# Optimization experiments

Hardware: AMD Instinct MI355X
Metric: run time of the kernel (lower is better)

## Reference

```python
import jax, jax.numpy as jnp
import numpy as np

DMODEL = 512
NUM_HEADS = 8
HEAD_DIM = DMODEL // NUM_HEADS
ATTN_LEN = 5
BATCH = 4
SEQ = 4096


def kv_roll(t, layer, shift):
    # t: [B, h_sub, T, 1, hd]; replicates tf.pad + tf.roll + concat + slice
    T = t.shape[2]
    dil = 2 ** layer
    p = dil * (ATTN_LEN // 2)
    tp = jnp.pad(t, ((0, 0), (0, 0), (p, p), (0, 0), (0, 0)))
    # circular rolls, concat along the singleton window axis -> [B,h,T+2p,ATTN_LEN,hd]
    rolled = jnp.concatenate(
        [jnp.roll(tp, -i * dil, axis=2) for i in range(shift, ATTN_LEN + shift)],
        axis=3,
    )
    return rolled[:, :, :T]


def setup_inputs() -> dict:
    key = jax.random.key(0)
    ks = jax.random.split(key, 8)
    inputs = jax.random.normal(ks[0], (BATCH, SEQ, DMODEL), dtype=jnp.float32)
    Wq = jax.random.normal(ks[1], (DMODEL, DMODEL), dtype=jnp.float32) * 0.02
    bq = jnp.zeros((DMODEL,), dtype=jnp.float32)
    Wk = jax.random.normal(ks[2], (DMODEL, DMODEL), dtype=jnp.float32) * 0.02
    bk = jnp.zeros((DMODEL,), dtype=jnp.float32)
    Wv = jax.random.normal(ks[3], (DMODEL, DMODEL), dtype=jnp.float32) * 0.02
    bv = jnp.zeros((DMODEL,), dtype=jnp.float32)
    Er = jax.random.normal(ks[4], (NUM_HEADS, HEAD_DIM, ATTN_LEN), dtype=jnp.float32) * 0.05
    return {"inputs": inputs, "Wq": Wq, "bq": bq, "Wk": Wk, "bk": bk,
            "Wv": Wv, "bv": bv, "Er": Er, "layer": 1}


def reference(inputs, Wq, bq, Wk, bk, Wv, bv, Er, layer):
    B, T, D = inputs.shape
    # projections -> [B, H, T, 1, hd]
    def proj(W, b):
        x = inputs @ W + b
        x = x.reshape(B, T, NUM_HEADS, 1, HEAD_DIM)
        return jnp.transpose(x, (0, 2, 1, 3, 4))
    q = proj(Wq, bq)
    k = proj(Wk, bk)
    v = proj(Wv, bv)

    def build_windows(t):
        # per-head-group shifts: heads 0-3 shift 0, head 4 shift -2, head 5 -1, head 6 +1, head 7 +2
        return jnp.concatenate((
            kv_roll(t[:, 0:4], layer, 0),
            kv_roll(t[:, 4:5], layer, -2),
            kv_roll(t[:, 5:6], layer, -1),
            kv_roll(t[:, 6:7], layer, 1),
            kv_roll(t[:, 7:8], layer, 2),
        ), axis=1)  # [B, H, T, ATTN_LEN, hd]

    kw = build_windows(k)
    vw = build_windows(v)

    # qk: [B, H, T, 1, ATTN_LEN]
    qk = jnp.einsum('bhtqd,bhtwd->bhtqw', q, kw)
    # relative positional bias: q @ Er -> [B, H, T, 1, ATTN_LEN]
    qEr = jnp.einsum('bhtqd,hdw->bhtqw', q, Er)
    scale = jnp.sqrt(jnp.float32(HEAD_DIM)).astype(inputs.dtype)
    logits = (qk + qEr) / scale
    mask = (qk == 0).astype(logits.dtype)
    attn = jax.nn.softmax(logits + mask * -10000.0, axis=-1)
    # out: [B, H, T, 1, hd]
    out = jnp.einsum('bhtqw,bhtwd->bhtqd', attn, vw)
    out = jnp.transpose(out[:, :, :, 0, :], (0, 2, 1, 3)).reshape(B, T, D)
    return out, attn
```

## Files before the change

### kernel.cpp

```cpp
#include <hip/hip_runtime.h>
#include <stdint.h>

#define B_ 4
#define T_ 4096
#define D_ 512
#define H_ 8
#define HD_ 64
#define W_ 5
#define M_ (B_*T_)
#define TILE 128
#define HALO 16
#define TMg 160
#define TN 192
#define LSTR 72

#define AS1_OFF 5120
#define BS0_OFF 10240
#define BS1_OFF 16384
#define SH_ELEMS 32256

typedef __attribute__((ext_vector_type(8))) short short8;
typedef __attribute__((ext_vector_type(4))) float floatx4;

__device__ __forceinline__ unsigned short f2bf(float f) {
    unsigned int u = __builtin_bit_cast(unsigned int, f);
    u += 0x7fffu + ((u >> 16) & 1u);
    return (unsigned short)(u >> 16);
}
__device__ __forceinline__ float bf2f(unsigned short s) {
    unsigned int u = ((unsigned int)s) << 16;
    return __builtin_bit_cast(float, u);
}
__device__ __forceinline__ void load8bf(const unsigned short* p, float* f) {
    uint4 d = *(const uint4*)p;
    f[0] = bf2f((unsigned short)(d.x & 0xffffu));
    f[1] = bf2f((unsigned short)(d.x >> 16));
    f[2] = bf2f((unsigned short)(d.y & 0xffffu));
    f[3] = bf2f((unsigned short)(d.y >> 16));
    f[4] = bf2f((unsigned short)(d.z & 0xffffu));
    f[5] = bf2f((unsigned short)(d.z >> 16));
    f[6] = bf2f((unsigned short)(d.w & 0xffffu));
    f[7] = bf2f((unsigned short)(d.w >> 16));
}

__device__ __forceinline__ void async16(const unsigned short* g, unsigned short* l) {
    __builtin_amdgcn_global_load_lds(
        (const __attribute__((address_space(1))) unsigned int*)g,
        (__attribute__((address_space(3))) unsigned int*)l, 16, 0, 0);
}

__global__ __launch_bounds__(256) void prep(const float* __restrict__ x,
                                            const float* __restrict__ Wq,
                                            const float* __restrict__ Wk,
                                            const float* __restrict__ Wv,
                                            unsigned short* __restrict__ xb,
                                            unsigned short* __restrict__ Wt2) {
    int bx = blockIdx.x;
    if (bx < 4096) {
        int i = bx * 256 + threadIdx.x;
        const float4* x4 = (const float4*)x;
        float4 a = x4[2*i], b = x4[2*i + 1];
        uint4 o;
        o.x = (unsigned)f2bf(a.x) | ((unsigned)f2bf(a.y) << 16);
        o.y = (unsigned)f2bf(a.z) | ((unsigned)f2bf(a.w) << 16);
        o.z = (unsigned)f2bf(b.x) | ((unsigned)f2bf(b.y) << 16);
        o.w = (unsigned)f2bf(b.z) | ((unsigned)f2bf(b.w) << 16);
        ((uint4*)xb)[i] = o;
    } else {
        int tid = (bx - 4096) * 256 + threadIdx.x;
        int np = tid % 1536;
        int kc = tid / 1536;
        int h = np / 192, n192 = np % 192;
        int sel = n192 >> 6, ch = n192 & 63;
        int c = h * 64 + ch;
        const float* Wsrc = (sel == 0) ? Wq : ((sel == 1) ? Wk : Wv);
        unsigned short us[8];
#pragma unroll
        for (int j = 0; j < 8; j++)
            us[j] = f2bf(Wsrc[(size_t)(kc*8 + j) * D_ + c]);
        uint4 o;
        o.x = (unsigned)us[0] | ((unsigned)us[1] << 16);
        o.y = (unsigned)us[2] | ((unsigned)us[3] << 16);
        o.z = (unsigned)us[4] | ((unsigned)us[5] << 16);
        o.w = (unsigned)us[6] | ((unsigned)us[7] << 16);
        *(uint4*)(Wt2 + (size_t)np * D_ + kc*8) = o;
    }
}

__global__ __launch_bounds__(512, 4) void fused_qkv_attn(
    const unsigned short* __restrict__ Xb,
    const unsigned short* __restrict__ Wt2,
    const float* __restrict__ bq, const float* __restrict__ bk2,
    const float* __restrict__ bv, const float* __restrict__ Er,
    const int* __restrict__ layer_p,
    float* __restrict__ out,
    float* __restrict__ attn_out)
{
    __shared__ unsigned short SH[SH_ELEMS];
    __shared__ float sEr[HD_ * W_];
    unsigned short* As0 = SH;
    unsigned short* Bs0 = SH + BS0_OFF;
    unsigned short* Qs = SH;
    unsigned short* Ks = SH + TILE * LSTR;
    unsigned short* Vs = SH + (TILE + TMg) * LSTR;

    const int tid = threadIdx.x;
    const int wave = tid >> 6, lane = tid & 63;
    const int tile = blockIdx.x >> 3, h = blockIdx.x & 7;
    const int b = tile >> 5;
    const int t0 = (tile & 31) * TILE;
    const long m0g = (long)b * T_ + t0;

    for (int i = tid; i < HD_ * W_; i += 512)
        sEr[i] = Er[h * HD_ * W_ + i];

    const unsigned short* gsrc[3];
    unsigned short* ldst[3];
    int halfoff[3];
#pragma unroll
    for (int j = 0; j < 3; j++) {
        int q = wave + j * 8;
        if (q < 22) {
            if (q < 10) {
                long grow = m0g - HALO + q*16 + (lane >> 2);
                grow = grow < 0 ? 0 : (grow >= M_ ? M_ - 1 : grow);
                gsrc[j] = Xb + grow * D_ + (lane & 3) * 8;
                ldst[j] = As0 + q * 512;
                halfoff[j] = AS1_OFF;
            } else {
                int q2 = q - 10;
                gsrc[j] = Wt2 + ((size_t)h*TN + q2*16 + (lane >> 2)) * D_ + (lane & 3) * 8;
                ldst[j] = Bs0 + q2 * 512;
                halfoff[j] = BS1_OFF - BS0_OFF;
            }
        }
    }

    const int wm = (wave >> 2) * 80;
    const int wn = (wave & 3) * 48;
    const int qd = lane >> 4, r16 = lane & 15;
    floatx4 acc[5][3] = {};

    for (int kc = 0; kc < D_; kc += 64) {
#pragma unroll
        for (int j = 0; j < 3; j++)
            if (wave + j * 8 < 22) {
                async16(gsrc[j] + kc,      ldst[j]);
                async16(gsrc[j] + kc + 32, ldst[j] + halfoff[j]);
            }
        __syncthreads();
        short8 af[5][2], bf[3][2];
#pragma unroll
        for (int half = 0; half < 2; half++) {
            const unsigned short* Ab = SH + half * AS1_OFF;
            const unsigned short* Bb = SH + BS0_OFF + half * (BS1_OFF - BS0_OFF);
#pragma unroll
            for (int mi = 0; mi < 5; mi++)
                af[mi][half] = __builtin_bit_cast(short8,
                    *(const uint4*)(Ab + (wm + mi*16 + r16)*32 + qd*8));
#pragma unroll
            for (int ni = 0; ni < 3; ni++)
                bf[ni][half] = __builtin_bit_cast(short8,
                    *(const uint4*)(Bb + (wn + ni*16 + r16)*32 + qd*8));
        }
#pragma unroll
        for (int half = 0; half < 2; half++)
#pragma unroll
            for (int mi = 0; mi < 5; mi++)
#pragma unroll
                for (int ni = 0; ni < 3; ni++)
                    acc[mi][ni] = __builtin_amdgcn_mfma_f32_16x16x32_bf16(
                        af[mi][half], bf[ni][half], acc[mi][ni], 0, 0, 0);
        __syncthreads();
    }

#pragma unroll
    for (int ni = 0; ni < 3; ni++) {
        int n192 = wn + ni * 16 + r16;
        int sel = n192 >> 6;
        int ch = n192 & 63;
        float bias = (sel == 0) ? bq[h*64 + ch]
                   : (sel == 1) ? bk2[h*64 + ch] : bv[h*64 + ch];
#pragma unroll
        for (int mi = 0; mi < 5; mi++)
#pragma unroll
            for (int r = 0; r < 4; r++) {
                int l = wm + mi*16 + qd*4 + r;
                unsigned short vb = f2bf(acc[mi][ni][r] + bias);
                if (sel == 0) {
                    if (l >= HALO && l < HALO + TILE)
                        Qs[(l - HALO) * LSTR + ch] = vb;
                } else if (sel == 1) {
                    Ks[l * LSTR + ch] = vb;
                } else {
                    Vs[l * LSTR + ch] = vb;
                }
            }
    }
    __syncthreads();

    const int dil = 1 << layer_p[0];
    const int sh = (h < 4) ? 0 : (h == 4 ? -2 : (h == 5 ? -1 : (h == 6 ? 1 : 2)));
    const int c8 = tid & 7, g64 = tid >> 3;

#pragma unroll
    for (int p = 0; p < 2; p++) {
        int tl = g64 + p * 64;
        int t = t0 + tl;
        float qf[8]; load8bf(Qs + tl * LSTR + c8 * 8, qf);

        int pos[W_]; bool val[W_]; float s[W_];
#pragma unroll
        for (int w = 0; w < W_; w++) {
            pos[w] = t + (sh + w - 2) * dil;
            val[w] = (pos[w] >= 0) && (pos[w] < T_);
            float a = 0.f;
            if (val[w]) {
                float kf[8]; load8bf(Ks + (pos[w] - t0 + HALO) * LSTR + c8 * 8, kf);
#pragma unroll
                for (int j = 0; j < 8; j++) a = fmaf(qf[j], kf[j], a);
            }
#pragma unroll
            for (int j = 0; j < 8; j++)
                a = fmaf(qf[j], sEr[(c8*8 + j) * W_ + w], a);
            s[w] = a;
        }
#pragma unroll
        for (int off = 4; off > 0; off >>= 1)
#pragma unroll
            for (int w = 0; w < W_; w++)
                s[w] += __shfl_xor(s[w], off, 8);

        float logit[W_], mx = -1e30f;
#pragma unroll
        for (int w = 0; w < W_; w++) {
            logit[w] = val[w] ? s[w] * 0.125f : -1e30f;
            mx = fmaxf(mx, logit[w]);
        }
        float pw[W_], ssum = 0.f;
#pragma unroll
        for (int w = 0; w < W_; w++) {
            pw[w] = val[w] ? __expf(logit[w] - mx) : 0.f;
            ssum += pw[w];
        }
        const float inv = 1.f / ssum;
        float aw[W_];
#pragma unroll
        for (int w = 0; w < W_; w++) aw[w] = pw[w] * inv;

        if (c8 < W_)
            attn_out[((size_t)(b * H_ + h) * T_ + t) * W_ + c8] = aw[c8];

        float of[8] = {0,0,0,0,0,0,0,0};
#pragma unroll
        for (int w = 0; w < W_; w++) {
            if (val[w]) {
                float vf[8]; load8bf(Vs + (pos[w] - t0 + HALO) * LSTR + c8 * 8, vf);
#pragma unroll
                for (int j = 0; j < 8; j++) of[j] = fmaf(aw[w], vf[j], of[j]);
            }
        }
        float* orow = out + ((size_t)b * T_ + t) * D_ + h * HD_ + c8 * 8;
        *(float4*)(orow)     = make_float4(of[0], of[1], of[2], of[3]);
        *(float4*)(orow + 4) = make_float4(of[4], of[5], of[6], of[7]);
    }
}

extern "C" void kernel_launch(void* const* d_in, const int* in_sizes, int n_in,
                              void* d_out, int out_size, void* d_ws, size_t ws_size,
                              hipStream_t stream) {
    const float* x   = (const float*)d_in[0];
    const float* Wq  = (const float*)d_in[1];
    const float* bq  = (const float*)d_in[2];
    const float* Wk  = (const float*)d_in[3];
    const float* bk  = (const float*)d_in[4];
    const float* Wv  = (const float*)d_in[5];
    const float* bv  = (const float*)d_in[6];
    const float* Er  = (const float*)d_in[7];
    const int* layer = (const int*)d_in[8];

    char* ws = (char*)d_ws;
    unsigned short* Xb  = (unsigned short*)ws;
    unsigned short* Wt2 = (unsigned short*)(ws + (size_t)16*1024*1024);

    float* out  = (float*)d_out;
    float* attn = out + (size_t)B_ * T_ * D_;

    prep<<<4096 + 384, 256, 0, stream>>>(x, Wq, Wk, Wv, Xb, Wt2);
    fused_qkv_attn<<<(M_ / TILE) * 8, 512, 0, stream>>>(Xb, Wt2, bq, bk, bv,
                                                        Er, layer, out, attn);
}
```

Baseline: 149.4 us.

## Double-buffer activation tiles in LDS and load weight fragments directly from global

The GEMM main loop now double-buffers only the activation (A) tile in shared memory, prefetching the next K-chunk while the current one is consumed. It also drops shared-memory staging of the weight (B) tile: each wave reads its MFMA B fragments straight from global memory. This halves the barriers per iteration and overlaps the async copies with compute, at the cost of more global/L2 traffic for the weights, which several blocks reuse, and possible exposed global-load latency.

```diff
diff --git a/kernel.cpp b/kernel.cpp
--- a/kernel.cpp
+++ b/kernel.cpp
@@ -14,9 +14,8 @@
 #define TN 192
 #define LSTR 72
 
-#define AS1_OFF 5120
-#define BS0_OFF 10240
-#define BS1_OFF 16384
+#define AHALF 5120
+#define ABUF  10240
 #define SH_ELEMS 32256
 
 typedef __attribute__((ext_vector_type(8))) short short8;
@@ -98,8 +97,6 @@
 {
     __shared__ unsigned short SH[SH_ELEMS];
     __shared__ float sEr[HD_ * W_];
-    unsigned short* As0 = SH;
-    unsigned short* Bs0 = SH + BS0_OFF;
     unsigned short* Qs = SH;
     unsigned short* Ks = SH + TILE * LSTR;
     unsigned short* Vs = SH + (TILE + TMg) * LSTR;
@@ -114,63 +111,70 @@
     for (int i = tid; i < HD_ * W_; i += 512)
         sEr[i] = Er[h * HD_ * W_ + i];
 
-    const unsigned short* gsrc[3];
-    unsigned short* ldst[3];
-    int halfoff[3];
+    const unsigned short* agA[3];
+    unsigned short* alA[3];
+    int nA = 0;
 #pragma unroll
     for (int j = 0; j < 3; j++) {
-        int q = wave + j * 8;
-        if (q < 22) {
-            if (q < 10) {
-                long grow = m0g - HALO + q*16 + (lane >> 2);
-                grow = grow < 0 ? 0 : (grow >= M_ ? M_ - 1 : grow);
-                gsrc[j] = Xb + grow * D_ + (lane & 3) * 8;
-                ldst[j] = As0 + q * 512;
-                halfoff[j] = AS1_OFF;
-            } else {
-                int q2 = q - 10;
-                gsrc[j] = Wt2 + ((size_t)h*TN + q2*16 + (lane >> 2)) * D_ + (lane & 3) * 8;
-                ldst[j] = Bs0 + q2 * 512;
-                halfoff[j] = BS1_OFF - BS0_OFF;
-            }
-        }
-    }
-
-    const int wm = (wave >> 2) * 80;
-    const int wn = (wave & 3) * 48;
+        int J = wave + 8 * j;
+        if (J < 20) {
+            int q = J >> 1, hh = J & 1;
+            long grow = m0g - HALO + q*16 + (lane >> 2);
+            grow = grow < 0 ? 0 : (grow >= M_ ? M_ - 1 : grow);
+            agA[nA] = Xb + grow * D_ + hh*32 + (lane & 3) * 8;
+            alA[nA] = SH + hh * AHALF + q * 512 + lane * 8;
+            nA++;
+        }
+    }
+
+    const int wm = (wave >> 2) * 80, wn = (wave & 3) * 48;
     const int qd = lane >> 4, r16 = lane & 15;
+    const unsigned short* bsrc[3];
+#pragma unroll
+    for (int ni = 0; ni < 3; ni++)
+        bsrc[ni] = Wt2 + ((size_t)(h * TN + wn + ni*16 + r16)) * D_ + qd * 8;
+
+#pragma unroll
+    for (int j = 0; j < 3; j++)
+        if (j < nA) async16(agA[j], alA[j]);
+    __syncthreads();
+
     floatx4 acc[5][3] = {};
 
-    for (int kc = 0; kc < D_; kc += 64) {
-#pragma unroll
-        for (int j = 0; j < 3; j++)
-            if (wave + j * 8 < 22) {
-                async16(gsrc[j] + kc,      ldst[j]);
-                async16(gsrc[j] + kc + 32, ldst[j] + halfoff[j]);
-            }
-        __syncthreads();
-        short8 af[5][2], bf[3][2];
-#pragma unroll
-        for (int half = 0; half < 2; half++) {
-            const unsigned short* Ab = SH + half * AS1_OFF;
-            const unsigned short* Bb = SH + BS0_OFF + half * (BS1_OFF - BS0_OFF);
+#pragma unroll
+    for (int it = 0; it < 8; it++) {
+        const int kc = it * 64;
+        const unsigned short* Abuf = SH + (it & 1) * ABUF;
+
+        short8 bf[2][3];
+#pragma unroll
+        for (int hh = 0; hh < 2; hh++)
+#pragma unroll
+            for (int ni = 0; ni < 3; ni++)
+                bf[hh][ni] = __builtin_bit_cast(short8,
+                    *(const uint4*)(bsrc[ni] + kc + hh*32));
+
+        if (it < 7) {
+#pragma unroll
+            for (int j = 0; j < 3; j++)
+                if (j < nA)
+                    async16(agA[j] + kc + 64, alA[j] + ((it + 1) & 1) * ABUF);
+        }
+
+#pragma unroll
+        for (int hh = 0; hh < 2; hh++) {
+            short8 af[5];
 #pragma unroll
             for (int mi = 0; mi < 5; mi++)
-                af[mi][half] = __builtin_bit_cast(short8,
-                    *(const uint4*)(Ab + (wm + mi*16 + r16)*32 + qd*8));
-#pragma unroll
-            for (int ni = 0; ni < 3; ni++)
-                bf[ni][half] = __builtin_bit_cast(short8,
-                    *(const uint4*)(Bb + (wn + ni*16 + r16)*32 + qd*8));
-        }
-#pragma unroll
-        for (int half = 0; half < 2; half++)
+                af[mi] = __builtin_bit_cast(short8,
+                    *(const uint4*)(Abuf + hh*AHALF + (wm + mi*16 + r16)*32 + qd*8));
 #pragma unroll
             for (int mi = 0; mi < 5; mi++)
 #pragma unroll
                 for (int ni = 0; ni < 3; ni++)
                     acc[mi][ni] = __builtin_amdgcn_mfma_f32_16x16x32_bf16(
-                        af[mi][half], bf[ni][half], acc[mi][ni], 0, 0, 0);
+                        af[mi], bf[hh][ni], acc[mi][ni], 0, 0, 0);
+        }
         __syncthreads();
     }
 
```

Result: slower. 186.6 us (+24.9%).
